# Performance work log

Measured on AMD Instinct MI355X. Metric: run time of the kernel, lower is better.

The kernel has to match this reference:

```python
import jax, jax.numpy as jnp
import numpy as np

B, T, DIM = 1, 1024, 1024
H = 8
QLR, KVLR = 768, 512
DNOPE, DROPE, DV = 128, 64, 128
DK = DNOPE + DROPE  # 192
EPS = 1e-5


def _rms(x, w):
    return x * jax.lax.rsqrt(jnp.mean(x * x, axis=-1, keepdims=True) + EPS) * w


def _l2norm(x):
    return x * jax.lax.rsqrt(jnp.sum(x * x, axis=-1, keepdims=True) + 1e-6)


def setup_inputs() -> dict:
    key = jax.random.key(0)
    ks = jax.random.split(key, 12)
    std = 0.02
    rnd = lambda k, shape: (jax.random.normal(k, shape, dtype=jnp.float32) * std)
    return {
        'x': jax.random.normal(ks[0], (B, T, DIM), dtype=jnp.float32),
        'cos': jax.random.normal(ks[1], (T, DROPE), dtype=jnp.float32),
        'sin': jax.random.normal(ks[2], (T, DROPE), dtype=jnp.float32),
        'wq_a': rnd(ks[3], (DIM, QLR)),
        'q_norm_w': jnp.ones((QLR,), dtype=jnp.float32),
        'wq_b': rnd(ks[4], (QLR, H * DK)),
        'wkv_a': rnd(ks[5], (DIM, KVLR + DROPE)),
        'kv_norm_w': jnp.ones((KVLR,), dtype=jnp.float32),
        'wkv_b': rnd(ks[6], (KVLR, H * (DNOPE + DV))),
        'wg_w': rnd(ks[7], (DIM, H * DK)),
        'wg_b': jnp.zeros((H * DK,), dtype=jnp.float32),
        'wb': rnd(ks[8], (DIM, H)),
        'wo': rnd(ks[9], (H * DV, DIM)),
    }


def _kda(q, k, v, g, beta):
    # q,k: [B,T,H,DK]; v: [B,T,H,DV]; g: [B,T,H,DK] (log-decay); beta: [B,T,H]
    q = _l2norm(q) * (DK ** -0.5)
    k = _l2norm(k)
    # time-major for scan
    qs = jnp.moveaxis(q, 1, 0)
    ks_ = jnp.moveaxis(k, 1, 0)
    vs = jnp.moveaxis(v, 1, 0)
    gs = jnp.moveaxis(g, 1, 0)
    bs = jnp.moveaxis(beta, 1, 0)

    def step(S, inp):
        q_t, k_t, v_t, g_t, b_t = inp  # [B,H,DK],[B,H,DK],[B,H,DV],[B,H,DK],[B,H]
        S = S * jnp.exp(g_t)[..., None]                       # per-key-dim decay
        u_t = b_t[..., None] * (v_t - jnp.einsum('bhk,bhkv->bhv', k_t, S))
        S = S + k_t[..., None] * u_t[..., None, :]            # rank-1 delta update
        o_t = jnp.einsum('bhk,bhkv->bhv', q_t, S)
        return S, o_t

    S0 = jnp.zeros((B, H, DK, DV), dtype=q.dtype)
    _, o = jax.lax.scan(step, S0, (qs, ks_, vs, gs, bs))
    return jnp.moveaxis(o, 0, 1)  # [B,T,H,DV]


def reference(x, cos, sin, wq_a, q_norm_w, wq_b, wkv_a, kv_norm_w, wkv_b, wg_w, wg_b, wb, wo):
    # cos/sin are accepted but unused, matching the original forward body.
    q = (_rms(x @ wq_a, q_norm_w) @ wq_b).reshape(B, T, H, DK)
    kv_all = x @ wkv_a
    kv_c, k_pe = kv_all[..., :KVLR], kv_all[..., KVLR:]       # [B,T,KVLR],[B,T,DROPE]
    kv = (_rms(kv_c, kv_norm_w) @ wkv_b).reshape(B, T, H, DNOPE + DV)
    k_nope, v = kv[..., :DNOPE], kv[..., DNOPE:]
    k = jnp.concatenate(
        [k_nope, jnp.broadcast_to(k_pe[:, :, None, :], (B, T, H, DROPE))], axis=-1)
    g = jax.nn.log_sigmoid(x @ wg_w + wg_b).reshape(B, T, H, DK)
    beta = jax.nn.sigmoid(x @ wb).reshape(B, T, H)
    o = _kda(q, k, v, g, beta)
    o = jnp.nan_to_num(o, nan=0.0, posinf=10000.0, neginf=-10000.0)
    return o.reshape(B, T, H * DV) @ wo
```

## Files before the change

kernel.cpp:

```cpp
#include <hip/hip_runtime.h>
#include <hip/hip_bf16.h>
#include <math.h>

#define TT 1024
#define DIM 1024
#define HH 8
#define QLR 768
#define KVLR 512
#define DNOPE 128
#define DROPE 64
#define DV 128
#define DK 192
#define HDK (HH*DK)
#define HKV (HH*(DNOPE+DV))

#define OY   0
#define OQ   3072
#define OC   6144
#define OPL  9984
#define OU   10240
#define OLAM 12288
#define PABLK 12480

typedef __attribute__((ext_vector_type(8))) short short8;
typedef __attribute__((ext_vector_type(4))) float f32x4;

__device__ __forceinline__ unsigned short f2bf_rn(float f) {
    unsigned u = __float_as_uint(f);
    unsigned lsb = (u >> 16) & 1u;
    u += 0x7fffu + lsb;
    return (unsigned short)(u >> 16);
}
__device__ __forceinline__ float bf2f(unsigned short h) {
    return __uint_as_float(((unsigned)h) << 16);
}

__global__ __launch_bounds__(256) void wconv(
    const float* __restrict__ W0, unsigned short* __restrict__ H0,
    unsigned short* __restrict__ L0, int K0, int N0, int T0,
    const float* __restrict__ W1, unsigned short* __restrict__ H1,
    unsigned short* __restrict__ L1, int K1, int N1, int T1,
    const float* __restrict__ W2, unsigned short* __restrict__ H2,
    unsigned short* __restrict__ L2, int K2, int N2, int T2)
{
    __shared__ float Ls[64][65];
    int bx = blockIdx.x;
    const float* W; unsigned short* H; unsigned short* L; int K, N;
    if (bx < T0)           { W = W0; H = H0; L = L0; K = K0; N = N0; }
    else if (bx < T0 + T1) { bx -= T0; W = W1; H = H1; L = L1; K = K1; N = N1; }
    else                   { bx -= T0 + T1; W = W2; H = H2; L = L2; K = K2; N = N2; }

    const int NT = N >> 6;
    const int kt = bx / NT, nt = bx - kt * NT;
    const int k0 = kt * 64, n0 = nt * 64;
    const int tid = threadIdx.x;
    const int r = tid >> 2, c = (tid & 3) * 16;

#pragma unroll
    for (int i = 0; i < 4; i++)
        *(float4*)&Ls[r][c + i * 4] =
            *(const float4*)&W[(size_t)(k0 + r) * N + n0 + c + i * 4];
    __syncthreads();

    const int nr = tid >> 2, kc = (tid & 3) * 16;
    unsigned short hb[16], lb[16];
#pragma unroll
    for (int j = 0; j < 16; j++) {
        float v = Ls[kc + j][nr];
        unsigned short h = f2bf_rn(v);
        hb[j] = h;
        lb[j] = f2bf_rn(v - bf2f(h));
    }
    size_t ob = (size_t)(n0 + nr) * K + k0 + kc;
    *(float4*)&H[ob]     = ((float4*)hb)[0];
    *(float4*)&H[ob + 8] = ((float4*)hb)[1];
    *(float4*)&L[ob]     = ((float4*)lb)[0];
    *(float4*)&L[ob + 8] = ((float4*)lb)[1];
}

__global__ __launch_bounds__(256) void aconv(
    const float* __restrict__ A, unsigned short* __restrict__ H,
    unsigned short* __restrict__ L)
{
    int i = (blockIdx.x * 256 + threadIdx.x) * 8;
    float4 v0 = *(const float4*)&A[i];
    float4 v1 = *(const float4*)&A[i + 4];
    float vv[8] = {v0.x, v0.y, v0.z, v0.w, v1.x, v1.y, v1.z, v1.w};
    unsigned short hb[8], lb[8];
#pragma unroll
    for (int j = 0; j < 8; j++) {
        unsigned short h = f2bf_rn(vv[j]);
        hb[j] = h;
        lb[j] = f2bf_rn(vv[j] - bf2f(h));
    }
    *(float4*)&H[i] = *(float4*)hb;
    *(float4*)&L[i] = *(float4*)lb;
}

__global__ __launch_bounds__(128) void gemm_bt(
    const unsigned short* __restrict__ Ah0, const unsigned short* __restrict__ Al0,
    const unsigned short* __restrict__ Bh0, const unsigned short* __restrict__ Bl0,
    float* __restrict__ C0, int K0, int N0, int T0,
    const unsigned short* __restrict__ Ah1, const unsigned short* __restrict__ Al1,
    const unsigned short* __restrict__ Bh1, const unsigned short* __restrict__ Bl1,
    float* __restrict__ C1, int K1, int N1, int T1,
    const unsigned short* __restrict__ Ah2, const unsigned short* __restrict__ Al2,
    const unsigned short* __restrict__ Bh2, const unsigned short* __restrict__ Bl2,
    float* __restrict__ C2, int K2, int N2, int T2)
{
    __shared__ unsigned short Ahs[64 * 40], Als[64 * 40];
    __shared__ unsigned short Bhs[64 * 40], Bls[64 * 40];

    int bx = blockIdx.x;
    const unsigned short *Ah, *Al, *Bh, *Bl; float* C; int K, N;
    if (bx < T0) {
        Ah = Ah0; Al = Al0; Bh = Bh0; Bl = Bl0; C = C0; K = K0; N = N0;
    } else if (bx < T0 + T1) {
        bx -= T0; Ah = Ah1; Al = Al1; Bh = Bh1; Bl = Bl1; C = C1; K = K1; N = N1;
    } else {
        bx -= T0 + T1; Ah = Ah2; Al = Al2; Bh = Bh2; Bl = Bl2; C = C2; K = K2; N = N2;
    }

    const int tid = threadIdx.x;
    const int w = tid >> 6, l = tid & 63;
    const int q = l >> 4, m16 = l & 15;
    const int bm = blockIdx.y * 64, bn = bx * 64;

    const int c0i = tid * 2, c1i = tid * 2 + 1;
    const int r0 = c0i >> 2, o0 = (c0i & 3) * 8;
    const int r1 = c1i >> 2, o1 = (c1i & 3) * 8;
    const unsigned short* pAh0 = Ah + (size_t)(bm + r0) * K + o0;
    const unsigned short* pAh1 = Ah + (size_t)(bm + r1) * K + o1;
    const unsigned short* pAl0 = Al + (size_t)(bm + r0) * K + o0;
    const unsigned short* pAl1 = Al + (size_t)(bm + r1) * K + o1;
    const unsigned short* pBh0 = Bh + (size_t)(bn + r0) * K + o0;
    const unsigned short* pBh1 = Bh + (size_t)(bn + r1) * K + o1;
    const unsigned short* pBl0 = Bl + (size_t)(bn + r0) * K + o0;
    const unsigned short* pBl1 = Bl + (size_t)(bn + r1) * K + o1;

    f32x4 acc[2][4];
#pragma unroll
    for (int i = 0; i < 2; i++)
#pragma unroll
        for (int j = 0; j < 4; j++)
            acc[i][j] = (f32x4){0.f, 0.f, 0.f, 0.f};

    float4 vAh0 = *(const float4*)pAh0, vAh1 = *(const float4*)pAh1;
    float4 vAl0 = *(const float4*)pAl0, vAl1 = *(const float4*)pAl1;
    float4 vBh0 = *(const float4*)pBh0, vBh1 = *(const float4*)pBh1;
    float4 vBl0 = *(const float4*)pBl0, vBl1 = *(const float4*)pBl1;

    for (int k0 = 0;; k0 += 32) {
        __syncthreads();
        *(float4*)&Ahs[r0 * 40 + o0] = vAh0; *(float4*)&Ahs[r1 * 40 + o1] = vAh1;
        *(float4*)&Als[r0 * 40 + o0] = vAl0; *(float4*)&Als[r1 * 40 + o1] = vAl1;
        *(float4*)&Bhs[r0 * 40 + o0] = vBh0; *(float4*)&Bhs[r1 * 40 + o1] = vBh1;
        *(float4*)&Bls[r0 * 40 + o0] = vBl0; *(float4*)&Bls[r1 * 40 + o1] = vBl1;
        __syncthreads();

        const bool more = (k0 + 32) < K;
        if (more) {
            const int kn = k0 + 32;
            vAh0 = *(const float4*)(pAh0 + kn); vAh1 = *(const float4*)(pAh1 + kn);
            vAl0 = *(const float4*)(pAl0 + kn); vAl1 = *(const float4*)(pAl1 + kn);
            vBh0 = *(const float4*)(pBh0 + kn); vBh1 = *(const float4*)(pBh1 + kn);
            vBl0 = *(const float4*)(pBl0 + kn); vBl1 = *(const float4*)(pBl1 + kn);
        }

        short8 fah[2], fal[2], fbh[4], fbl[4];
#pragma unroll
        for (int mt = 0; mt < 2; mt++) {
            const int row = w * 32 + mt * 16 + m16;
            fah[mt] = *(const short8*)&Ahs[row * 40 + q * 8];
            fal[mt] = *(const short8*)&Als[row * 40 + q * 8];
        }
#pragma unroll
        for (int nt = 0; nt < 4; nt++) {
            const int row = nt * 16 + m16;
            fbh[nt] = *(const short8*)&Bhs[row * 40 + q * 8];
            fbl[nt] = *(const short8*)&Bls[row * 40 + q * 8];
        }
#pragma unroll
        for (int mt = 0; mt < 2; mt++)
#pragma unroll
            for (int nt = 0; nt < 4; nt++) {
                acc[mt][nt] = __builtin_amdgcn_mfma_f32_16x16x32_bf16(
                    fah[mt], fbh[nt], acc[mt][nt], 0, 0, 0);
                acc[mt][nt] = __builtin_amdgcn_mfma_f32_16x16x32_bf16(
                    fah[mt], fbl[nt], acc[mt][nt], 0, 0, 0);
                acc[mt][nt] = __builtin_amdgcn_mfma_f32_16x16x32_bf16(
                    fal[mt], fbh[nt], acc[mt][nt], 0, 0, 0);
            }
        if (!more) break;
    }

#pragma unroll
    for (int mt = 0; mt < 2; mt++)
#pragma unroll
        for (int nt = 0; nt < 4; nt++) {
            const int mrow = bm + w * 32 + mt * 16 + q * 4;
            const int ncol = bn + nt * 16 + m16;
#pragma unroll
            for (int r = 0; r < 4; r++)
                C[(size_t)(mrow + r) * N + ncol] = acc[mt][nt][r];
        }
}

__global__ __launch_bounds__(256) void rmsnorm_bf2(
    const float* __restrict__ in0, const float* __restrict__ w0,
    unsigned short* __restrict__ oh0, unsigned short* __restrict__ ol0,
    const float* __restrict__ in1, const float* __restrict__ w1,
    unsigned short* __restrict__ oh1, unsigned short* __restrict__ ol1)
{
    int bx = blockIdx.x;
    const float* in; const float* w; unsigned short *oh, *ol;
    int t, stride, ncols; float inv_n;
    if (bx < TT) {
        t = bx; in = in0; w = w0; oh = oh0; ol = ol0;
        stride = QLR; ncols = QLR; inv_n = 1.f / QLR;
    } else {
        t = bx - TT; in = in1; w = w1; oh = oh1; ol = ol1;
        stride = KVLR + DROPE; ncols = KVLR; inv_n = 1.f / KVLR;
    }
    const int tid = threadIdx.x;
    const float* row = in + (size_t)t * stride;
    float ss = 0.f;
    for (int c = tid; c < ncols; c += 256) { float v = row[c]; ss += v * v; }
#pragma unroll
    for (int m = 1; m < 64; m <<= 1) ss += __shfl_xor(ss, m);
    __shared__ float red[4];
    if ((tid & 63) == 0) red[tid >> 6] = ss;
    __syncthreads();
    float tot = red[0] + red[1] + red[2] + red[3];
    float scale = rsqrtf(tot * inv_n + 1e-5f);
    for (int c = tid; c < ncols; c += 256) {
        float v = row[c] * scale * w[c];
        unsigned short h = f2bf_rn(v);
        oh[(size_t)t * ncols + c] = h;
        ol[(size_t)t * ncols + c] = f2bf_rn(v - bf2f(h));
    }
}

__global__ __launch_bounds__(256) void small_fused(
    const float* __restrict__ g, const float* __restrict__ bias,
    float* __restrict__ la_h,
    const float* __restrict__ x, const float* __restrict__ wb,
    float* __restrict__ betab,
    const float* __restrict__ qraw, const float* __restrict__ kvb,
    const float* __restrict__ kv_all, float* __restrict__ q_h,
    float* __restrict__ k_h)
{
    int bx = blockIdx.x;
    if (bx < 6144) {
        int i = bx * 256 + threadIdx.x;
        int t = i / HDK, col = i - t * HDK;
        int h = col / DK, d = col - h * DK;
        float z = g[i] + bias[col];
        float la = fminf(z, 0.f) - log1pf(__expf(-fabsf(z)));
        la_h[((size_t)h * TT + t) * DK + d] = la;
        return;
    }
    bx -= 6144;
    const int lane = threadIdx.x & 63, wv = threadIdx.x >> 6;
    if (bx < 2048) {
        const int p = bx * 4 + wv;
        const int t = p >> 3, h = p & 7;
        const float* xr = x + (size_t)t * DIM;
        float s = 0.f;
        for (int e = lane; e < DIM; e += 64) s += xr[e] * wb[e * HH + h];
#pragma unroll
        for (int m = 1; m < 64; m <<= 1) s += __shfl_xor(s, m);
        if (lane == 0) betab[p] = 1.f / (1.f + expf(-s));
        return;
    }
    bx -= 2048;
    {
        const int p = bx * 4 + wv;
        const int t = p >> 3, h = p & 7;

        const float* qrow = qraw + (size_t)t * HDK + h * DK;
        float q0 = qrow[lane], q1 = qrow[lane + 64], q2 = qrow[lane + 128];
        float ss = q0 * q0 + q1 * q1 + q2 * q2;
#pragma unroll
        for (int m = 1; m < 64; m <<= 1) ss += __shfl_xor(ss, m);
        float sc = rsqrtf(ss + 1e-6f) * 0.07216878364870323f;
        float* qo = q_h + ((size_t)h * TT + t) * DK;
        qo[lane] = q0 * sc; qo[lane + 64] = q1 * sc; qo[lane + 128] = q2 * sc;

        const float* knope = kvb + (size_t)t * HKV + h * (DNOPE + DV);
        float k0 = knope[lane], k1 = knope[lane + 64];
        float k2 = kv_all[(size_t)t * (KVLR + DROPE) + KVLR + lane];
        float ks = k0 * k0 + k1 * k1 + k2 * k2;
#pragma unroll
        for (int m = 1; m < 64; m <<= 1) ks += __shfl_xor(ks, m);
        float kc = rsqrtf(ks + 1e-6f);
        float* ko = k_h + ((size_t)h * TT + t) * DK;
        ko[lane] = k0 * kc; ko[lane + 64] = k1 * kc; ko[lane + 128] = k2 * kc;
    }
}

__device__ __forceinline__ float dpp_xor1(float x) {
    return __int_as_float(__builtin_amdgcn_update_dpp(
        0, __float_as_int(x), 0xB1, 0xF, 0xF, false));
}
__device__ __forceinline__ float dpp_xor2(float x) {
    return __int_as_float(__builtin_amdgcn_update_dpp(
        0, __float_as_int(x), 0x4E, 0xF, 0xF, false));
}
__device__ __forceinline__ float dpp_hm(float x) {
    return __int_as_float(__builtin_amdgcn_update_dpp(
        0, __float_as_int(x), 0x141, 0xF, 0xF, false));
}
__device__ __forceinline__ float red16(float x) {
    x += dpp_xor1(x);
    x += dpp_xor2(x);
    x += dpp_hm(x);
    x += __int_as_float(__builtin_amdgcn_update_dpp(0, __float_as_int(x), 0x140, 0xF, 0xF, false));
    return x;
}
__device__ __forceinline__ float red8(float x) {
    x += dpp_xor1(x);
    x += dpp_xor2(x);
    x += dpp_hm(x);
    return x;
}

__device__ __forceinline__ void gl_lds16(const float* g, float* l) {
    __builtin_amdgcn_global_load_lds(
        (const __attribute__((address_space(1))) void*)g,
        (__attribute__((address_space(3))) void*)l, 16, 0, 0);
}
__device__ __forceinline__ void gl_lds4(const float* g, float* l) {
    __builtin_amdgcn_global_load_lds(
        (const __attribute__((address_space(1))) void*)g,
        (__attribute__((address_space(3))) void*)l, 4, 0, 0);
}

__global__ __launch_bounds__(256) void chunk_prep(
    const float* __restrict__ k_h, const float* __restrict__ la_h,
    const float* __restrict__ q_h, const float* __restrict__ kvb,
    const float* __restrict__ betab, float* __restrict__ pa)
{
    __shared__ float Ls[16][196];
    __shared__ float Ks[16][196];
    __shared__ float Qs[16][196];
    __shared__ float Ws[16][196];
    __shared__ float Xs[16][196];
    __shared__ float Ms[16][16];
    __shared__ float bs[16];

    const int tid = threadIdx.x;
    const int n = blockIdx.x >> 3, h = blockIdx.x & 7;
    const size_t g0 = ((size_t)h * TT + n * 16) * DK;
    float* blob = pa + (size_t)blockIdx.x * PABLK;

#pragma unroll
    for (int s = 0; s < 3; s++) {
        int off = (tid * 3 + s) * 4;
        int r = off / 192, c = off - r * 192;
        *(float4*)&Ks[r][c] = *(const float4*)(k_h + g0 + off);
        *(float4*)&Ls[r][c] = *(const float4*)(la_h + g0 + off);
        *(float4*)&Qs[r][c] = *(const float4*)(q_h + g0 + off);
    }
    if (tid < 16) bs[tid] = betab[(size_t)(n * 16 + tid) * HH + h];
    __syncthreads();

    if (tid < 192) {
        float g = 0.f;
#pragma unroll
        for (int i = 0; i < 16; i++) { g += Ls[i][tid]; Ls[i][tid] = g; }
    }
    __syncthreads();

#pragma unroll
    for (int s = 0; s < 12; s++) {
        int idx = s * 256 + tid;
        int i = idx / 192, d = idx - i * 192;
        float G = Ls[i][d];
        float eg = __expf(G), en = __expf(-G);
        float kk = Ks[i][d];
        Ws[i][d] = bs[i] * kk * eg;
        Qs[i][d] *= eg;
        Ks[i][d] = kk * en;
    }
    __syncthreads();

#pragma unroll
    for (int s = 0; s < 3; s++) {
        int off = (tid * 3 + s) * 4;
        int r = off / 192, c = off - r * 192;
        *(float4*)(blob + OQ + off) = *(const float4*)&Qs[r][c];
    }
    if (tid < 192) {
        float lam = __expf(Ls[15][tid]);
        blob[OLAM + tid] = lam;
#pragma unroll
        for (int j4 = 0; j4 < 4; j4++) {
            float4 v;
            v.x = Ks[j4 * 4 + 0][tid] * lam; v.y = Ks[j4 * 4 + 1][tid] * lam;
            v.z = Ks[j4 * 4 + 2][tid] * lam; v.w = Ks[j4 * 4 + 3][tid] * lam;
            *(float4*)(blob + OC + tid * 20 + j4 * 4) = v;
        }
        blob[OC + tid * 20 + 16] = 0.f; blob[OC + tid * 20 + 17] = 0.f;
        blob[OC + tid * 20 + 18] = 0.f; blob[OC + tid * 20 + 19] = 0.f;
    }
    {
        const int i = tid >> 4, j = tid & 15;
        float m = 0.f, p = 0.f;
#pragma unroll
        for (int d4 = 0; d4 < 48; d4++) {
            float4 w  = *(const float4*)&Ws[i][d4 * 4];
            float4 ka = *(const float4*)&Ks[j][d4 * 4];
            float4 qa = *(const float4*)&Qs[i][d4 * 4];
            m += w.x * ka.x + w.y * ka.y + w.z * ka.z + w.w * ka.w;
            p += qa.x * ka.x + qa.y * ka.y + qa.z * ka.z + qa.w * ka.w;
        }
        Ms[i][j] = (j < i) ? m : 0.f;
        blob[OPL + tid] = (j <= i) ? p : 0.f;
    }
    __syncthreads();

    float y[16], uu[16];
    const bool doY = (tid < 192);
    const bool doU = (tid >= 128);
    const int dcol = tid, ccol = tid - 128;
    if (doY) {
#pragma unroll
        for (int i = 0; i < 16; i++) y[i] = Ws[i][dcol];
#pragma unroll
        for (int i = 1; i < 16; i++)
#pragma unroll
            for (int j = 0; j < i; j++)
                y[i] = fmaf(-Ms[i][j], y[j], y[i]);
    }
    if (doU) {
#pragma unroll
        for (int i = 0; i < 16; i++)
            uu[i] = bs[i] * kvb[(size_t)(n * 16 + i) * HKV + h * (DNOPE + DV) + DNOPE + ccol];
#pragma unroll
        for (int i = 1; i < 16; i++)
#pragma unroll
            for (int j = 0; j < i; j++)
                uu[i] = fmaf(-Ms[i][j], uu[j], uu[i]);
    }
    if (doY) {
#pragma unroll
        for (int i = 0; i < 16; i++) Xs[i][dcol] = y[i];
    }
    __syncthreads();
#pragma unroll
    for (int s = 0; s < 3; s++) {
        int off = (tid * 3 + s) * 4;
        int r = off / 192, c = off - r * 192;
        *(float4*)(blob + OY + off) = *(const float4*)&Xs[r][c];
    }
    __syncthreads();
    if (doU) {
#pragma unroll
        for (int i = 0; i < 16; i++) Xs[i][ccol] = uu[i];
    }
    __syncthreads();
#pragma unroll
    for (int s = 0; s < 2; s++) {
        int off = (tid * 2 + s) * 4;
        int r = off / 128, c = off - r * 128;
        *(float4*)(blob + OU + off) = *(const float4*)&Xs[r][c];
    }
}

__global__ __launch_bounds__(256) void kda_chunk(
    const float* __restrict__ pa, unsigned short* __restrict__ obh,
    unsigned short* __restrict__ obl)
{
    __shared__ float Cb[3][3840];
    __shared__ float Pb[3][256];
    __shared__ float ubs[3][32];
    __shared__ float lbs[3][192];
    __shared__ float Ss[392];
    __shared__ float us[40];

    const int tid = threadIdx.x;
    const int w = tid >> 6, lane = tid & 63;
    const int h = blockIdx.x >> 6, cg = blockIdx.x & 63;
    const int c0 = cg * 2;

    const int dg  = tid & 15;
    const int cc  = (tid >> 4) & 1;
    const int tig = tid >> 5;
    const int dbase = dg * 12;

    auto stage = [&](int buf, int n) {
        const float* blob = pa + (size_t)(n * 8 + h) * PABLK;
        if (w == 0) {
#pragma unroll
            for (int s = 0; s < 8; s++)
                gl_lds16(blob + OC + s * 256 + lane * 4, &Cb[buf][s * 256]);
        } else if (w == 1) {
#pragma unroll
            for (int s = 8; s < 15; s++)
                gl_lds16(blob + OC + s * 256 + lane * 4, &Cb[buf][s * 256]);
        } else if (w == 2) {
            gl_lds16(blob + OPL + lane * 4, &Pb[buf][0]);
            if (lane < 32)
                gl_lds4(blob + OU + (lane >> 1) * 128 + c0 + (lane & 1), &ubs[buf][0]);
            if (lane < 48)
                gl_lds16(blob + OLAM + lane * 4, &lbs[buf][0]);
        }
    };

    auto ldYQ = [&](int n, float4 (&Y)[2][3], float4 (&Q)[2][3]) {
        const float* blob = pa + (size_t)(n * 8 + h) * PABLK;
#pragma unroll
        for (int i = 0; i < 2; i++) {
            const float* py = blob + OY + (tig * 2 + i) * 192 + dbase;
            const float* pq = blob + OQ + (tig * 2 + i) * 192 + dbase;
#pragma unroll
            for (int s = 0; s < 3; s++) {
                Y[i][s] = *(const float4*)(py + s * 4);
                Q[i][s] = *(const float4*)(pq + s * 4);
            }
        }
    };

    for (int idx = tid; idx < 392; idx += 256) Ss[idx] = 0.f;
    stage(0, 0);
    stage(1, 1);

    float4 YA[2][3], QA[2][3], YB[2][3], QB[2][3];
    ldYQ(0, YA, QA);

    const int c2 = tid & 1, dseg = tid >> 1;

    auto body = [&](int n, int bf, float4 (&Yc)[2][3], float4 (&Qc)[2][3],
                    float4 (&Yn)[2][3], float4 (&Qn)[2][3]) {
        __syncthreads();

        if (n + 2 < TT / 16) {
            int b2 = bf + 2; if (b2 >= 3) b2 -= 3;
            stage(b2, n + 2);
        }
        {
            int np = n + 1; if (np > TT / 16 - 1) np = TT / 16 - 1;
            ldYQ(np, Yn, Qn);
        }

        float4 sv[3];
#pragma unroll
        for (int s = 0; s < 3; s++)
            sv[s] = *(const float4*)&Ss[cc * 196 + dbase + s * 4];

        float py[2] = {0.f, 0.f};
        float pq[2] = {0.f, 0.f};
#pragma unroll
        for (int i = 0; i < 2; i++)
#pragma unroll
            for (int s = 0; s < 3; s++) {
                float4 yv = Yc[i][s];
                float4 qv = Qc[i][s];
                float4 s4 = sv[s];
                py[i] = fmaf(yv.x, s4.x, py[i]);
                py[i] = fmaf(yv.y, s4.y, py[i]);
                py[i] = fmaf(yv.z, s4.z, py[i]);
                py[i] = fmaf(yv.w, s4.w, py[i]);
                pq[i] = fmaf(qv.x, s4.x, pq[i]);
                pq[i] = fmaf(qv.y, s4.y, pq[i]);
                pq[i] = fmaf(qv.z, s4.z, pq[i]);
                pq[i] = fmaf(qv.w, s4.w, pq[i]);
            }
        float zy[2], zq[2];
#pragma unroll
        for (int i = 0; i < 2; i++) {
            zy[i] = red16(py[i]);
            zq[i] = red16(pq[i]);
        }

        float uv[2];
#pragma unroll
        for (int i = 0; i < 2; i++)
            uv[i] = ubs[bf][(tig * 2 + i) * 2 + cc] - zy[i];
        if ((dg & 7) == 0) {
            const int ii = dg >> 3;
            us[cc * 20 + tig * 2 + ii] = (ii == 0) ? uv[0] : uv[1];
        }
        __syncthreads();

        {
            const int ii = dg >> 3, qtr = dg & 7;
            const int ti = tig * 2 + ii;
            float acc = 0.f;
#pragma unroll
            for (int j = qtr; j <= 15; j += 8)
                if (j <= ti) acc = fmaf(Pb[bf][ti * 16 + j], us[cc * 20 + j], acc);
            acc = red8(acc);
            if (qtr == 0) {
                float ov = zq[ii] + acc;
                if (isnan(ov)) ov = 0.f;
                else if (isinf(ov)) ov = ov > 0.f ? 1e4f : -1e4f;
                size_t oi = (size_t)(n * 16 + ti) * (HH * DV) + h * DV + c0 + cc;
                unsigned short hb = f2bf_rn(ov);
                obh[oi] = hb;
                obl[oi] = f2bf_rn(ov - bf2f(hb));
            }
        }

        if (tid < 128) {
            const float4* up = (const float4*)&us[c2 * 20];
            float4 u0 = up[0], u1 = up[1], u2v = up[2], u3 = up[3];
#pragma unroll
            for (int s = 0; s < 3; s++) {
                int d = dseg * 3 + s;
                float svv = Ss[c2 * 196 + d];
                float a2 = lbs[bf][d] * svv;
                const float4* C4 = (const float4*)&Cb[bf][d * 20];
                float4 k0 = C4[0], k1 = C4[1], k2 = C4[2], k3 = C4[3];
                a2 = fmaf(k0.x, u0.x,  a2); a2 = fmaf(k0.y, u0.y,  a2);
                a2 = fmaf(k0.z, u0.z,  a2); a2 = fmaf(k0.w, u0.w,  a2);
                a2 = fmaf(k1.x, u1.x,  a2); a2 = fmaf(k1.y, u1.y,  a2);
                a2 = fmaf(k1.z, u1.z,  a2); a2 = fmaf(k1.w, u1.w,  a2);
                a2 = fmaf(k2.x, u2v.x, a2); a2 = fmaf(k2.y, u2v.y, a2);
                a2 = fmaf(k2.z, u2v.z, a2); a2 = fmaf(k2.w, u2v.w, a2);
                a2 = fmaf(k3.x, u3.x,  a2); a2 = fmaf(k3.y, u3.y,  a2);
                a2 = fmaf(k3.z, u3.z,  a2); a2 = fmaf(k3.w, u3.w,  a2);
                Ss[c2 * 196 + d] = a2;
            }
        }
    };

    int buf = 0;
    for (int n = 0; n < TT / 16; n += 2) {
        body(n, buf, YA, QA, YB, QB);
        int b1 = buf + 1; if (b1 >= 3) b1 -= 3;
        body(n + 1, b1, YB, QB, YA, QA);
        buf += 2; if (buf >= 3) buf -= 3;
    }
}

extern "C" void kernel_launch(void* const* d_in, const int* in_sizes, int n_in,
                              void* d_out, int out_size, void* d_ws, size_t ws_size,
                              hipStream_t stream)
{
    const float* x         = (const float*)d_in[0];
    const float* wq_a      = (const float*)d_in[3];
    const float* q_norm_w  = (const float*)d_in[4];
    const float* wq_b      = (const float*)d_in[5];
    const float* wkv_a     = (const float*)d_in[6];
    const float* kv_norm_w = (const float*)d_in[7];
    const float* wkv_b     = (const float*)d_in[8];
    const float* wg_w      = (const float*)d_in[9];
    const float* wg_b      = (const float*)d_in[10];
    const float* wb        = (const float*)d_in[11];
    const float* wo        = (const float*)d_in[12];
    float* out = (float*)d_out;

    float* ws = (float*)d_ws;
    float* xq     = ws;
    float* kv_all = xq     + TT * QLR;
    float* agraw  = kv_all + TT * (KVLR + DROPE);
    float* qnraw  = agraw  + TT * HDK;
    float* kvb    = qnraw  + TT * HDK;
    float* la_h   = kvb    + TT * HKV;
    float* q_h    = la_h   + TT * HDK;
    float* k_h    = q_h    + TT * HDK;
    float* betab  = k_h    + TT * HDK;
    float* pa     = betab  + TT * HH;
    float* tail   = pa     + 512 * PABLK;

    unsigned short* wo_h  = (unsigned short*)tail;
    unsigned short* wo_l  = wo_h  + 1048576;
    unsigned short* xh    = wo_l  + 1048576;
    unsigned short* xl    = xh    + 1048576;
    unsigned short* xqh   = xl    + 1048576;
    unsigned short* xql   = xqh   + 786432;
    unsigned short* kvnh  = xql   + 786432;
    unsigned short* kvnl  = kvnh  + 524288;

    unsigned short* wqa_h  = (unsigned short*)pa;
    unsigned short* wqa_l  = wqa_h  + 786432;
    unsigned short* wkva_h = wqa_l  + 786432;
    unsigned short* wkva_l = wkva_h + 589824;
    unsigned short* wgw_h  = wkva_l + 589824;
    unsigned short* wgw_l  = wgw_h  + 1572864;
    unsigned short* wqb_h  = wgw_l  + 1572864;
    unsigned short* wqb_l  = wqb_h  + 1179648;
    unsigned short* wkvb_h = wqb_l  + 1179648;
    unsigned short* wkvb_l = wkvb_h + 1048576;

    unsigned short* obh = (unsigned short*)agraw;
    unsigned short* obl = obh + 1048576;

    dim3 blk(256);

    wconv<<<dim3(192 + 144 + 384), blk, 0, stream>>>(
        wq_a, wqa_h, wqa_l, DIM, QLR, 192,
        wkv_a, wkva_h, wkva_l, DIM, KVLR + DROPE, 144,
        wg_w, wgw_h, wgw_l, DIM, HDK, 384);
    wconv<<<dim3(288 + 256 + 256), blk, 0, stream>>>(
        wq_b, wqb_h, wqb_l, QLR, HDK, 288,
        wkv_b, wkvb_h, wkvb_l, KVLR, HKV, 256,
        wo, wo_h, wo_l, DIM, DIM, 256);

    aconv<<<dim3(TT * DIM / (256 * 8)), blk, 0, stream>>>(x, xh, xl);

    gemm_bt<<<dim3(12 + 9 + 24, 16), dim3(128), 0, stream>>>(
        xh, xl, wqa_h, wqa_l, xq, DIM, QLR, 12,
        xh, xl, wkva_h, wkva_l, kv_all, DIM, KVLR + DROPE, 9,
        xh, xl, wgw_h, wgw_l, agraw, DIM, HDK, 24);

    rmsnorm_bf2<<<dim3(2 * TT), blk, 0, stream>>>(
        xq, q_norm_w, xqh, xql,
        kv_all, kv_norm_w, kvnh, kvnl);

    gemm_bt<<<dim3(24 + 32, 16), dim3(128), 0, stream>>>(
        xqh, xql, wqb_h, wqb_l, qnraw, QLR, HDK, 24,
        kvnh, kvnl, wkvb_h, wkvb_l, kvb, KVLR, HKV, 32,
        xh, xl, wqa_h, wqa_l, xq, DIM, QLR, 0);

    small_fused<<<dim3(6144 + 2048 + 2048), blk, 0, stream>>>(
        agraw, wg_b, la_h,
        x, wb, betab,
        qnraw, kvb, kv_all, q_h, k_h);

    chunk_prep<<<512, blk, 0, stream>>>(k_h, la_h, q_h, kvb, betab, pa);
    kda_chunk<<<512, blk, 0, stream>>>(pa, obh, obl);

    gemm_bt<<<dim3(16, 16), dim3(128), 0, stream>>>(
        obh, obl, wo_h, wo_l, out, DIM, DIM, 16,
        xh, xl, wqa_h, wqa_l, xq, DIM, QLR, 0,
        xh, xl, wqa_h, wqa_l, xq, DIM, QLR, 0);
}
```

Baseline: 316.7 us.

## Load decay-scaled K rows directly to registers instead of LDS staging

Result: slower. 340.0 us (+7.4%).

```diff
diff --git a/kernel.cpp b/kernel.cpp
--- a/kernel.cpp
+++ b/kernel.cpp
@@ -401,7 +401,8 @@
             v.z = Ks[j4 * 4 + 2][tid] * lam; v.w = Ks[j4 * 4 + 3][tid] * lam;
             *(float4*)(blob + OC + tid * 20 + j4 * 4) = v;
         }
-        blob[OC + tid * 20 + 16] = 0.f; blob[OC + tid * 20 + 17] = 0.f;
+        blob[OC + tid * 20 + 16] = lam;
+        blob[OC + tid * 20 + 17] = 0.f;
         blob[OC + tid * 20 + 18] = 0.f; blob[OC + tid * 20 + 19] = 0.f;
     }
     {
@@ -472,10 +473,8 @@
     const float* __restrict__ pa, unsigned short* __restrict__ obh,
     unsigned short* __restrict__ obl)
 {
-    __shared__ float Cb[3][3840];
     __shared__ float Pb[3][256];
     __shared__ float ubs[3][32];
-    __shared__ float lbs[3][192];
     __shared__ float Ss[392];
     __shared__ float us[40];
 
@@ -492,56 +491,52 @@
     auto stage = [&](int buf, int n) {
         const float* blob = pa + (size_t)(n * 8 + h) * PABLK;
         if (w == 0) {
-#pragma unroll
-            for (int s = 0; s < 8; s++)
-                gl_lds16(blob + OC + s * 256 + lane * 4, &Cb[buf][s * 256]);
-        } else if (w == 1) {
-#pragma unroll
-            for (int s = 8; s < 15; s++)
-                gl_lds16(blob + OC + s * 256 + lane * 4, &Cb[buf][s * 256]);
-        } else if (w == 2) {
             gl_lds16(blob + OPL + lane * 4, &Pb[buf][0]);
             if (lane < 32)
                 gl_lds4(blob + OU + (lane >> 1) * 128 + c0 + (lane & 1), &ubs[buf][0]);
-            if (lane < 48)
-                gl_lds16(blob + OLAM + lane * 4, &lbs[buf][0]);
         }
     };
 
-    auto ldYQ = [&](int n, float4 (&Y)[2][3], float4 (&Q)[2][3]) {
+    for (int idx = tid; idx < 392; idx += 256) Ss[idx] = 0.f;
+    stage(0, 0);
+    stage(1, 1);
+
+    const int c2 = tid & 1, dseg = tid >> 1;
+    const bool upd = (tid < 192);
+
+    int buf = 0;
+    for (int n = 0; n < TT / 16; n++) {
+        __syncthreads();
+
+        if (n + 2 < TT / 16) {
+            int b2 = buf + 2; if (b2 >= 3) b2 -= 3;
+            stage(b2, n + 2);
+        }
+
         const float* blob = pa + (size_t)(n * 8 + h) * PABLK;
+
+        float4 cb0[4], cb1[4]; float lam0 = 0.f, lam1 = 0.f;
+        if (upd) {
+            const float* cp0 = blob + OC + (dseg * 2 + 0) * 20;
+            const float* cp1 = blob + OC + (dseg * 2 + 1) * 20;
+            cb0[0] = *(const float4*)(cp0);      cb0[1] = *(const float4*)(cp0 + 4);
+            cb0[2] = *(const float4*)(cp0 + 8);  cb0[3] = *(const float4*)(cp0 + 12);
+            lam0 = cp0[16];
+            cb1[0] = *(const float4*)(cp1);      cb1[1] = *(const float4*)(cp1 + 4);
+            cb1[2] = *(const float4*)(cp1 + 8);  cb1[3] = *(const float4*)(cp1 + 12);
+            lam1 = cp1[16];
+        }
+
+        float4 Yc[2][3], Qc[2][3];
 #pragma unroll
         for (int i = 0; i < 2; i++) {
             const float* py = blob + OY + (tig * 2 + i) * 192 + dbase;
             const float* pq = blob + OQ + (tig * 2 + i) * 192 + dbase;
 #pragma unroll
             for (int s = 0; s < 3; s++) {
-                Y[i][s] = *(const float4*)(py + s * 4);
-                Q[i][s] = *(const float4*)(pq + s * 4);
+                Yc[i][s] = *(const float4*)(py + s * 4);
+                Qc[i][s] = *(const float4*)(pq + s * 4);
             }
-        }
-    };
-
-    for (int idx = tid; idx < 392; idx += 256) Ss[idx] = 0.f;
-    stage(0, 0);
-    stage(1, 1);
-
-    float4 YA[2][3], QA[2][3], YB[2][3], QB[2][3];
-    ldYQ(0, YA, QA);
-
-    const int c2 = tid & 1, dseg = tid >> 1;
-
-    auto body = [&](int n, int bf, float4 (&Yc)[2][3], float4 (&Qc)[2][3],
-                    float4 (&Yn)[2][3], float4 (&Qn)[2][3]) {
-        __syncthreads();
-
-        if (n + 2 < TT / 16) {
-            int b2 = bf + 2; if (b2 >= 3) b2 -= 3;
-            stage(b2, n + 2);
-        }
-        {
-            int np = n + 1; if (np > TT / 16 - 1) np = TT / 16 - 1;
-            ldYQ(np, Yn, Qn);
         }
 
         float4 sv[3];
@@ -549,8 +544,8 @@
         for (int s = 0; s < 3; s++)
             sv[s] = *(const float4*)&Ss[cc * 196 + dbase + s * 4];
 
-        float py[2] = {0.f, 0.f};
-        float pq[2] = {0.f, 0.f};
+        float py_[2] = {0.f, 0.f};
+        float pq_[2] = {0.f, 0.f};
 #pragma unroll
         for (int i = 0; i < 2; i++)
 #pragma unroll
@@ -558,26 +553,26 @@
                 float4 yv = Yc[i][s];
                 float4 qv = Qc[i][s];
                 float4 s4 = sv[s];
-                py[i] = fmaf(yv.x, s4.x, py[i]);
-                py[i] = fmaf(yv.y, s4.y, py[i]);
-                py[i] = fmaf(yv.z, s4.z, py[i]);
-                py[i] = fmaf(yv.w, s4.w, py[i]);
-                pq[i] = fmaf(qv.x, s4.x, pq[i]);
-                pq[i] = fmaf(qv.y, s4.y, pq[i]);
-                pq[i] = fmaf(qv.z, s4.z, pq[i]);
-                pq[i] = fmaf(qv.w, s4.w, pq[i]);
+                py_[i] = fmaf(yv.x, s4.x, py_[i]);
+                py_[i] = fmaf(yv.y, s4.y, py_[i]);
+                py_[i] = fmaf(yv.z, s4.z, py_[i]);
+                py_[i] = fmaf(yv.w, s4.w, py_[i]);
+                pq_[i] = fmaf(qv.x, s4.x, pq_[i]);
+                pq_[i] = fmaf(qv.y, s4.y, pq_[i]);
+                pq_[i] = fmaf(qv.z, s4.z, pq_[i]);
+                pq_[i] = fmaf(qv.w, s4.w, pq_[i]);
             }
         float zy[2], zq[2];
 #pragma unroll
         for (int i = 0; i < 2; i++) {
-            zy[i] = red16(py[i]);
-            zq[i] = red16(pq[i]);
+            zy[i] = red16(py_[i]);
+            zq[i] = red16(pq_[i]);
         }
 
         float uv[2];
 #pragma unroll
         for (int i = 0; i < 2; i++)
-            uv[i] = ubs[bf][(tig * 2 + i) * 2 + cc] - zy[i];
+            uv[i] = ubs[buf][(tig * 2 + i) * 2 + cc] - zy[i];
         if ((dg & 7) == 0) {
             const int ii = dg >> 3;
             us[cc * 20 + tig * 2 + ii] = (ii == 0) ? uv[0] : uv[1];
@@ -590,7 +585,7 @@
             float acc = 0.f;
 #pragma unroll
             for (int j = qtr; j <= 15; j += 8)
-                if (j <= ti) acc = fmaf(Pb[bf][ti * 16 + j], us[cc * 20 + j], acc);
+                if (j <= ti) acc = fmaf(Pb[buf][ti * 16 + j], us[cc * 20 + j], acc);
             acc = red8(acc);
             if (qtr == 0) {
                 float ov = zq[ii] + acc;
@@ -603,35 +598,36 @@
             }
         }
 
-        if (tid < 128) {
+        if (upd) {
             const float4* up = (const float4*)&us[c2 * 20];
             float4 u0 = up[0], u1 = up[1], u2v = up[2], u3 = up[3];
-#pragma unroll
-            for (int s = 0; s < 3; s++) {
-                int d = dseg * 3 + s;
-                float svv = Ss[c2 * 196 + d];
-                float a2 = lbs[bf][d] * svv;
-                const float4* C4 = (const float4*)&Cb[bf][d * 20];
-                float4 k0 = C4[0], k1 = C4[1], k2 = C4[2], k3 = C4[3];
-                a2 = fmaf(k0.x, u0.x,  a2); a2 = fmaf(k0.y, u0.y,  a2);
-                a2 = fmaf(k0.z, u0.z,  a2); a2 = fmaf(k0.w, u0.w,  a2);
-                a2 = fmaf(k1.x, u1.x,  a2); a2 = fmaf(k1.y, u1.y,  a2);
-                a2 = fmaf(k1.z, u1.z,  a2); a2 = fmaf(k1.w, u1.w,  a2);
-                a2 = fmaf(k2.x, u2v.x, a2); a2 = fmaf(k2.y, u2v.y, a2);
-                a2 = fmaf(k2.z, u2v.z, a2); a2 = fmaf(k2.w, u2v.w, a2);
-                a2 = fmaf(k3.x, u3.x,  a2); a2 = fmaf(k3.y, u3.y,  a2);
-                a2 = fmaf(k3.z, u3.z,  a2); a2 = fmaf(k3.w, u3.w,  a2);
-                Ss[c2 * 196 + d] = a2;
+            const int d0 = dseg * 2, d1 = d0 + 1;
+            {
+                float a2 = lam0 * Ss[c2 * 196 + d0];
+                a2 = fmaf(cb0[0].x, u0.x,  a2); a2 = fmaf(cb0[0].y, u0.y,  a2);
+                a2 = fmaf(cb0[0].z, u0.z,  a2); a2 = fmaf(cb0[0].w, u0.w,  a2);
+                a2 = fmaf(cb0[1].x, u1.x,  a2); a2 = fmaf(cb0[1].y, u1.y,  a2);
+                a2 = fmaf(cb0[1].z, u1.z,  a2); a2 = fmaf(cb0[1].w, u1.w,  a2);
+                a2 = fmaf(cb0[2].x, u2v.x, a2); a2 = fmaf(cb0[2].y, u2v.y, a2);
+                a2 = fmaf(cb0[2].z, u2v.z, a2); a2 = fmaf(cb0[2].w, u2v.w, a2);
+                a2 = fmaf(cb0[3].x, u3.x,  a2); a2 = fmaf(cb0[3].y, u3.y,  a2);
+                a2 = fmaf(cb0[3].z, u3.z,  a2); a2 = fmaf(cb0[3].w, u3.w,  a2);
+                Ss[c2 * 196 + d0] = a2;
             }
-        }
-    };
-
-    int buf = 0;
-    for (int n = 0; n < TT / 16; n += 2) {
-        body(n, buf, YA, QA, YB, QB);
-        int b1 = buf + 1; if (b1 >= 3) b1 -= 3;
-        body(n + 1, b1, YB, QB, YA, QA);
-        buf += 2; if (buf >= 3) buf -= 3;
+            {
+                float a2 = lam1 * Ss[c2 * 196 + d1];
+                a2 = fmaf(cb1[0].x, u0.x,  a2); a2 = fmaf(cb1[0].y, u0.y,  a2);
+                a2 = fmaf(cb1[0].z, u0.z,  a2); a2 = fmaf(cb1[0].w, u0.w,  a2);
+                a2 = fmaf(cb1[1].x, u1.x,  a2); a2 = fmaf(cb1[1].y, u1.y,  a2);
+                a2 = fmaf(cb1[1].z, u1.z,  a2); a2 = fmaf(cb1[1].w, u1.w,  a2);
+                a2 = fmaf(cb1[2].x, u2v.x, a2); a2 = fmaf(cb1[2].y, u2v.y, a2);
+                a2 = fmaf(cb1[2].z, u2v.z, a2); a2 = fmaf(cb1[2].w, u2v.w, a2);
+                a2 = fmaf(cb1[3].x, u3.x,  a2); a2 = fmaf(cb1[3].y, u3.y,  a2);
+                a2 = fmaf(cb1[3].z, u3.z,  a2); a2 = fmaf(cb1[3].w, u3.w,  a2);
+                Ss[c2 * 196 + d1] = a2;
+            }
+        }
+        buf = (buf + 1 == 3) ? 0 : buf + 1;
     }
 }
 
```
